# Kernel tuning notes

Measured on AMD Instinct MI355X. Metric: run time of the kernel, lower is better.

## Reference

```python
import jax, jax.numpy as jnp
import numpy as np

B, T, E = 4, 2048, 1024
H = 16
HS = E // H  # head_size = d_model // num_heads, d_model == E here
D_FF = 4 * E
EPS = 1e-5


def _layernorm(x, g, b):
    mu = jnp.mean(x, axis=-1, keepdims=True)
    var = jnp.var(x, axis=-1, keepdims=True)
    return (x - mu) * jax.lax.rsqrt(var + EPS) * g + b


def setup_inputs() -> dict:
    key = jax.random.key(0)
    ks = jax.random.split(key, 12)
    s_e = 1.0 / np.sqrt(E)
    s_ff = 1.0 / np.sqrt(D_FF)
    return {
        "x": jax.random.normal(ks[0], (B, T, E), jnp.float32),
        "ln1_g": jnp.ones((E,), jnp.float32),
        "ln1_b": jnp.zeros((E,), jnp.float32),
        "Wq": jax.random.normal(ks[1], (E, E), jnp.float32) * s_e,
        "bq": jnp.zeros((E,), jnp.float32),
        "Wk": jax.random.normal(ks[2], (E, E), jnp.float32) * s_e,
        "bk": jnp.zeros((E,), jnp.float32),
        "Wv": jax.random.normal(ks[3], (E, E), jnp.float32) * s_e,
        "bv": jnp.zeros((E,), jnp.float32),
        "Wp": jax.random.normal(ks[4], (E, E), jnp.float32) * s_e,
        "bp": jnp.zeros((E,), jnp.float32),
        "ln2_g": jnp.ones((E,), jnp.float32),
        "ln2_b": jnp.zeros((E,), jnp.float32),
        "W1": jax.random.normal(ks[5], (E, D_FF), jnp.float32) * s_e,
        "b1": jnp.zeros((D_FF,), jnp.float32),
        "W2": jax.random.normal(ks[6], (D_FF, E), jnp.float32) * s_ff,
        "b2": jnp.zeros((E,), jnp.float32),
    }


def reference(x, ln1_g, ln1_b, Wq, bq, Wk, bk, Wv, bv, Wp, bp,
              ln2_g, ln2_b, W1, b1, W2, b2):
    # --- attention sublayer ---
    h = _layernorm(x, ln1_g, ln1_b)                      # [B,T,E]
    q = (h @ Wq + bq).reshape(B, T, H, HS)
    k = (h @ Wk + bk).reshape(B, T, H, HS)
    v = (h @ Wv + bv).reshape(B, T, H, HS)
    scores = jnp.einsum('bqhd,bkhd->bhqk', q, k) * (HS ** -0.5)  # [B,H,T,T]
    causal = jnp.tril(jnp.ones((T, T), bool))
    scores = jnp.where(causal, scores, -jnp.inf)
    w = jax.nn.softmax(scores, axis=-1)
    attn = jnp.einsum('bhqk,bkhd->bqhd', w, v).reshape(B, T, H * HS)
    x = x + attn @ Wp + bp
    # --- FFN sublayer ---
    h2 = _layernorm(x, ln2_g, ln2_b)
    x = x + jax.nn.relu(h2 @ W1 + b1) @ W2 + b2
    return x
```

## Files before the change

### kernel.cpp

```cpp
#include <hip/hip_runtime.h>
#include <hip/hip_bf16.h>

#define B_ 4
#define T_ 2048
#define E_ 1024
#define H_ 16
#define HS_ 64
#define DFF_ 4096
#define M_ (B_ * T_)
#define LDQ_ (3 * E_)

typedef __bf16 bf16_t;
typedef __bf16 bf16x4 __attribute__((ext_vector_type(4)));
typedef __bf16 bf16x8 __attribute__((ext_vector_type(8)));
typedef float f32x4 __attribute__((ext_vector_type(4)));

#define AS1 __attribute__((address_space(1)))
#define AS3 __attribute__((address_space(3)))

__device__ __forceinline__ void gload_lds16(const void* g, void* l) {
  __builtin_amdgcn_global_load_lds((AS1 void*)(g), (AS3 void*)(l), 16, 0, 0);
}

__global__ __launch_bounds__(256) void wtrans_kernel(
    const float* __restrict__ W, bf16_t* __restrict__ Wt, int Krows, int Ncols) {
  __shared__ float tile[32][33];
  int tx = threadIdx.x, ty = threadIdx.y;
  int n0 = blockIdx.x * 32, k0 = blockIdx.y * 32;
#pragma unroll
  for (int i = 0; i < 32; i += 8)
    tile[ty + i][tx] = W[(long)(k0 + ty + i) * Ncols + n0 + tx];
  __syncthreads();
#pragma unroll
  for (int i = 0; i < 32; i += 8)
    Wt[(long)(n0 + ty + i) * Krows + k0 + tx] = (bf16_t)tile[tx][ty + i];
}

__global__ __launch_bounds__(256) void bcat_kernel(const float* a, const float* b,
                                                   const float* c, float* o) {
  int i = blockIdx.x * 256 + threadIdx.x;
  o[i] = i < 1024 ? a[i] : (i < 2048 ? b[i - 1024] : c[i - 2048]);
}

__global__ __launch_bounds__(256) void layernorm_kernel(
    const float* __restrict__ in, const float* __restrict__ g,
    const float* __restrict__ b, bf16_t* __restrict__ out) {
  int row = blockIdx.x;
  int tid = threadIdx.x;
  const float4* inr = (const float4*)(in + (long)row * E_);
  float4 v = inr[tid];
  float s = v.x + v.y + v.z + v.w;
  float ss = v.x * v.x + v.y * v.y + v.z * v.z + v.w * v.w;
#pragma unroll
  for (int o = 32; o; o >>= 1) {
    s += __shfl_xor(s, o);
    ss += __shfl_xor(ss, o);
  }
  __shared__ float red[8];
  int wv = tid >> 6;
  if ((tid & 63) == 0) {
    red[wv] = s;
    red[4 + wv] = ss;
  }
  __syncthreads();
  s = red[0] + red[1] + red[2] + red[3];
  ss = red[4] + red[5] + red[6] + red[7];
  float mu = s * (1.f / E_);
  float var = ss * (1.f / E_) - mu * mu;
  float rs = rsqrtf(var + 1e-5f);
  int ci = tid * 4;
  float4 gv = *(const float4*)(g + ci);
  float4 bv = *(const float4*)(b + ci);
  long o0 = (long)row * E_ + ci;
  out[o0 + 0] = (bf16_t)((v.x - mu) * rs * gv.x + bv.x);
  out[o0 + 1] = (bf16_t)((v.y - mu) * rs * gv.y + bv.y);
  out[o0 + 2] = (bf16_t)((v.z - mu) * rs * gv.z + bv.z);
  out[o0 + 3] = (bf16_t)((v.w - mu) * rs * gv.w + bv.w);
}

template <int RELU>
__global__ __launch_bounds__(512, 2) void gemm256_kernel(
    const bf16_t* __restrict__ A, const bf16_t* __restrict__ Bt,
    const float* __restrict__ bias, bf16_t* __restrict__ out, int N, int K) {
  __shared__ bf16_t As0[256 * 32], As1[256 * 32], As2[256 * 32], As3[256 * 32];
  __shared__ bf16_t Bs0[256 * 32], Bs1[256 * 32], Bs2[256 * 32], Bs3[256 * 32];
  const int tid = threadIdx.x;
  const int wave = tid >> 6;
  const int lane = tid & 63;
  const int wr = wave >> 2;
  const int wc = wave & 3;
  const int quad = lane >> 4, l16 = lane & 15;

  const int gx = gridDim.x;
  const int id = blockIdx.y * gx + blockIdx.x;
  const int xcd = id & 7;
  const int k_ = id >> 3;
  const int bxr = k_ % gx;
  const int byr = (k_ / gx) * 8 + xcd;
  const long rowBase = (long)byr * 256;
  const long colBase = (long)bxr * 256;

  f32x4 acc[8][4] = {};

  const int ntiles = K >> 5;

  auto stageA = [&](bf16_t* dst, int t) {
    const int k0 = t << 5;
#pragma unroll
    for (int p = 0; p < 2; ++p) {
      int idx = p * 512 + tid;
      int row = idx >> 2;
      int col = (idx & 3) * 8;
      gload_lds16(&A[(rowBase + row) * K + k0 + col],
                  dst + (p * 512 + wave * 64) * 8);
    }
  };
  auto stageB = [&](bf16_t* dst, int t) {
    const int k0 = t << 5;
#pragma unroll
    for (int p = 0; p < 2; ++p) {
      int idx = p * 512 + tid;
      int row = idx >> 2;
      int col = (idx & 3) * 8;
      gload_lds16(&Bt[(colBase + row) * K + k0 + col],
                  dst + (p * 512 + wave * 64) * 8);
    }
  };

  auto tileStep = [&](int t, const bf16_t* as, const bf16_t* bs, bf16_t* nA,
                      bf16_t* nB) {
    const bool pre = (t + 3 < ntiles);
    bf16x8 bfrag[4];
#pragma unroll
    for (int fc = 0; fc < 4; ++fc)
      bfrag[fc] = *(const bf16x8*)&bs[(wc * 64 + fc * 16 + l16) * 32 + quad * 8];

    {
      bf16x8 afrag[4];
#pragma unroll
      for (int fr = 0; fr < 4; ++fr)
        afrag[fr] =
            *(const bf16x8*)&as[(wr * 128 + fr * 16 + l16) * 32 + quad * 8];
      if (pre) stageA(nA, t + 3);
      __builtin_amdgcn_s_setprio(1);
#pragma unroll
      for (int fr = 0; fr < 4; ++fr)
#pragma unroll
        for (int fc = 0; fc < 4; ++fc)
          acc[fr][fc] = __builtin_amdgcn_mfma_f32_16x16x32_bf16(
              afrag[fr], bfrag[fc], acc[fr][fc], 0, 0, 0);
      __builtin_amdgcn_s_setprio(0);
      __builtin_amdgcn_s_barrier();
    }
    {
      bf16x8 afrag[4];
#pragma unroll
      for (int fr = 0; fr < 4; ++fr)
        afrag[fr] = *(const bf16x8*)&as[(wr * 128 + 64 + fr * 16 + l16) * 32 +
                                        quad * 8];
      if (pre) stageB(nB, t + 3);
      __builtin_amdgcn_s_setprio(1);
#pragma unroll
      for (int fr = 0; fr < 4; ++fr)
#pragma unroll
        for (int fc = 0; fc < 4; ++fc)
          acc[4 + fr][fc] = __builtin_amdgcn_mfma_f32_16x16x32_bf16(
              afrag[fr], bfrag[fc], acc[4 + fr][fc], 0, 0, 0);
      __builtin_amdgcn_s_setprio(0);
      if (t + 3 < ntiles)
        asm volatile("s_waitcnt vmcnt(8)" ::: "memory");
      else if (t + 2 < ntiles)
        asm volatile("s_waitcnt vmcnt(4)" ::: "memory");
      else if (t + 1 < ntiles)
        asm volatile("s_waitcnt vmcnt(0)" ::: "memory");
      if (t + 1 < ntiles) __builtin_amdgcn_s_barrier();
    }
  };

  stageA(As0, 0); stageB(Bs0, 0);
  stageA(As1, 1); stageB(Bs1, 1);
  stageA(As2, 2); stageB(Bs2, 2);
  asm volatile("s_waitcnt vmcnt(8)" ::: "memory");
  __builtin_amdgcn_s_barrier();

  for (int t = 0; t < ntiles; t += 4) {
    tileStep(t + 0, As0, Bs0, As3, Bs3);
    tileStep(t + 1, As1, Bs1, As0, Bs0);
    tileStep(t + 2, As2, Bs2, As1, Bs1);
    tileStep(t + 3, As3, Bs3, As2, Bs2);
  }

#pragma unroll
  for (int mh = 0; mh < 2; ++mh)
#pragma unroll
    for (int fr = 0; fr < 4; ++fr)
#pragma unroll
      for (int fc = 0; fc < 4; ++fc) {
        int colg = (int)colBase + wc * 64 + fc * 16 + l16;
        float bv = bias[colg];
#pragma unroll
        for (int r = 0; r < 4; ++r) {
          long rowg = rowBase + wr * 128 + mh * 64 + fr * 16 + quad * 4 + r;
          float v = acc[mh * 4 + fr][fc][r] + bv;
          if (RELU) v = fmaxf(v, 0.f);
          out[rowg * N + colg] = (bf16_t)v;
        }
      }
}

template <int MODE>
__global__ __launch_bounds__(512, 1) void gemm256x128_kernel(
    const bf16_t* __restrict__ A, const bf16_t* __restrict__ Bt,
    const float* __restrict__ bias, const float* __restrict__ resid,
    void* __restrict__ out, int N, int K) {
  __shared__ bf16_t As0[256 * 32], As1[256 * 32], As2[256 * 32], As3[256 * 32];
  __shared__ bf16_t Bs0[128 * 32], Bs1[128 * 32], Bs2[128 * 32], Bs3[128 * 32];
  const int tid = threadIdx.x;
  const int wave = tid >> 6;
  const int lane = tid & 63;
  const int wr = wave >> 1;
  const int wc = wave & 1;
  const int quad = lane >> 4, l16 = lane & 15;

  const int gx = gridDim.x;
  const int id = blockIdx.y * gx + blockIdx.x;
  const int xcd = id & 7;
  const int k_ = id >> 3;
  const int bxr = k_ % gx;
  const int byr = (k_ / gx) * 8 + xcd;
  const long rowBase = (long)byr * 256;
  const long colBase = (long)bxr * 128;

  f32x4 acc[4][4] = {};

  const int ntiles = K >> 5;

  auto stageA = [&](bf16_t* dst, int t) {
    const int k0 = t << 5;
#pragma unroll
    for (int p = 0; p < 2; ++p) {
      int idx = p * 512 + tid;
      int row = idx >> 2;
      int col = (idx & 3) * 8;
      gload_lds16(&A[(rowBase + row) * K + k0 + col],
                  dst + (p * 512 + wave * 64) * 8);
    }
  };
  auto stageB = [&](bf16_t* dst, int t) {
    const int k0 = t << 5;
    int row = tid >> 2;
    int col = (tid & 3) * 8;
    gload_lds16(&Bt[(colBase + row) * K + k0 + col], dst + (wave * 64) * 8);
  };

  auto tileStep = [&](int t, const bf16_t* as, const bf16_t* bs, bf16_t* nA,
                      bf16_t* nB) {
    const bool pre = (t + 3 < ntiles);
    bf16x8 bfrag[4];
#pragma unroll
    for (int fc = 0; fc < 4; ++fc)
      bfrag[fc] = *(const bf16x8*)&bs[(wc * 64 + fc * 16 + l16) * 32 + quad * 8];

    {
      bf16x8 afrag[2];
#pragma unroll
      for (int fr = 0; fr < 2; ++fr)
        afrag[fr] =
            *(const bf16x8*)&as[(wr * 64 + fr * 16 + l16) * 32 + quad * 8];
      if (pre) stageA(nA, t + 3);
      __builtin_amdgcn_s_setprio(1);
#pragma unroll
      for (int fr = 0; fr < 2; ++fr)
#pragma unroll
        for (int fc = 0; fc < 4; ++fc)
          acc[fr][fc] = __builtin_amdgcn_mfma_f32_16x16x32_bf16(
              afrag[fr], bfrag[fc], acc[fr][fc], 0, 0, 0);
      __builtin_amdgcn_s_setprio(0);
      __builtin_amdgcn_s_barrier();
    }
    {
      bf16x8 afrag[2];
#pragma unroll
      for (int fr = 2; fr < 4; ++fr)
        afrag[fr - 2] =
            *(const bf16x8*)&as[(wr * 64 + fr * 16 + l16) * 32 + quad * 8];
      if (pre) stageB(nB, t + 3);
      __builtin_amdgcn_s_setprio(1);
#pragma unroll
      for (int fr = 2; fr < 4; ++fr)
#pragma unroll
        for (int fc = 0; fc < 4; ++fc)
          acc[fr][fc] = __builtin_amdgcn_mfma_f32_16x16x32_bf16(
              afrag[fr - 2], bfrag[fc], acc[fr][fc], 0, 0, 0);
      __builtin_amdgcn_s_setprio(0);
      if (t + 3 < ntiles)
        asm volatile("s_waitcnt vmcnt(6)" ::: "memory");
      else if (t + 2 < ntiles)
        asm volatile("s_waitcnt vmcnt(3)" ::: "memory");
      else if (t + 1 < ntiles)
        asm volatile("s_waitcnt vmcnt(0)" ::: "memory");
      if (t + 1 < ntiles) __builtin_amdgcn_s_barrier();
    }
  };

  stageA(As0, 0); stageB(Bs0, 0);
  stageA(As1, 1); stageB(Bs1, 1);
  stageA(As2, 2); stageB(Bs2, 2);
  asm volatile("s_waitcnt vmcnt(6)" ::: "memory");
  __builtin_amdgcn_s_barrier();

  for (int t = 0; t < ntiles; t += 4) {
    tileStep(t + 0, As0, Bs0, As3, Bs3);
    tileStep(t + 1, As1, Bs1, As0, Bs0);
    tileStep(t + 2, As2, Bs2, As1, Bs1);
    tileStep(t + 3, As3, Bs3, As2, Bs2);
  }

#pragma unroll
  for (int fr = 0; fr < 4; ++fr)
#pragma unroll
    for (int fc = 0; fc < 4; ++fc) {
      int colg = (int)colBase + wc * 64 + fc * 16 + l16;
      float bv = bias[colg];
#pragma unroll
      for (int r = 0; r < 4; ++r) {
        long rowg = rowBase + wr * 64 + fr * 16 + quad * 4 + r;
        float v = acc[fr][fc][r] + bv;
        long idx = rowg * N + colg;
        if (MODE == 0) {
          ((bf16_t*)out)[idx] = (bf16_t)v;
        } else {
          ((float*)out)[idx] = v + resid[idx];
        }
      }
    }
}

__global__ __launch_bounds__(256) void vtrans_kernel(
    const bf16_t* __restrict__ qkv, bf16_t* __restrict__ vt) {
  __shared__ bf16_t tile[32][33];
  int tx = threadIdx.x, ty = threadIdx.y;
  int t0 = blockIdx.x * 32;
  int d0 = (blockIdx.y & 1) * 32;
  int bh = blockIdx.y >> 1;
  int b = bh >> 4, hh = bh & 15;
#pragma unroll
  for (int i = 0; i < 32; i += 8)
    tile[ty + i][tx] =
        qkv[(long)(b * T_ + t0 + ty + i) * LDQ_ + 2 * E_ + hh * HS_ + d0 + tx];
  __syncthreads();
#pragma unroll
  for (int i = 0; i < 32; i += 8)
    vt[((long)bh * HS_ + d0 + ty + i) * T_ + t0 + tx] = tile[tx][ty + i];
}

__global__ __launch_bounds__(256) void flash_attn_kernel(
    const bf16_t* __restrict__ qkv, const bf16_t* __restrict__ vt,
    bf16_t* __restrict__ attn, bf16_t* __restrict__ Opart,
    float* __restrict__ mlpart) {
  int gx = blockIdx.x;
  int ti = 0, sp = 0;
  for (int t = 0; t < 16; ++t) {
    int ns = t / 6 + 1;
    if (gx < ns) { ti = t; sp = gx; break; }
    gx -= ns;
  }
  const int nsplit = ti / 6 + 1;
  const int totIt = 2 * (ti + 1);
  const int jbeg = 12 * sp;
  const int jend = min(jbeg + 12, totIt);

  const int tid = threadIdx.x;
  const int lane = tid & 63, wave = tid >> 6;
  const int quad = lane >> 4, l16 = lane & 15;
  const int bh = blockIdx.y, b = bh >> 4, hh = bh & 15;
  const int q0 = ti * 128;
  const int qw = q0 + wave * 32;

  __shared__ __align__(16) bf16_t Ks[2][64 * 64];
  __shared__ __align__(16) bf16_t Vs[2][64 * 64];
  __shared__ __align__(16) bf16_t Ps[4][16 * 64];

  const bf16_t* qb = qkv;
  const bf16_t* kb = qkv + E_;

  bf16x8 aq[2][2];
#pragma unroll
  for (int s = 0; s < 2; ++s) {
    long base = (long)(b * T_ + qw + s * 16 + l16) * LDQ_ + hh * HS_ + quad * 8;
    aq[s][0] = *(const bf16x8*)&qb[base];
    aq[s][1] = *(const bf16x8*)&qb[base + 32];
#pragma unroll
    for (int e = 0; e < 8; ++e) {
      aq[s][0][e] = (bf16_t)((float)aq[s][0][e] * 0.125f);
      aq[s][1][e] = (bf16_t)((float)aq[s][1][e] * 0.125f);
    }
  }

  f32x4 o[2][4] = {};
  float lsum[2] = {};

  auto stage = [&](int buf, int j) {
    const int kv0 = j * 64;
#pragma unroll
    for (int i = 0; i < 2; ++i) {
      int c = i * 256 + tid;
      int row = c >> 3;
      int gcol = ((c & 7) ^ (row & 7)) * 8;
      gload_lds16(&kb[(long)(b * T_ + kv0 + row) * LDQ_ + hh * HS_ + gcol],
                  &Ks[buf][(i * 256 + wave * 64) * 8]);
      gload_lds16(&vt[((long)bh * HS_ + row) * T_ + kv0 + gcol],
                  &Vs[buf][(i * 256 + wave * 64) * 8]);
    }
  };

  stage(0, jbeg);
  __syncthreads();

  for (int j = jbeg; j < jend; ++j) {
    const int kv0 = j * 64;
    const int cur = (j - jbeg) & 1;
    if (j + 1 < jend) stage(cur ^ 1, j + 1);
    const bf16_t* KsL = Ks[cur];
    const bf16_t* VsL = Vs[cur];
    bf16_t* Pw = Ps[wave];

#pragma unroll
    for (int s = 0; s < 2; ++s) {
      const int qs = qw + s * 16;
      if (kv0 <= qs + 15) {
        f32x4 sc[4];
        __builtin_amdgcn_s_setprio(1);
#pragma unroll
        for (int sub = 0; sub < 4; ++sub) {
          const int rk = sub * 16 + l16;
          const int k0 = rk * 64 + ((quad ^ (rk & 7)) * 8);
          f32x4 t = {};
          t = __builtin_amdgcn_mfma_f32_16x16x32_bf16(
              *(const bf16x8*)&KsL[k0], aq[s][0], t, 0, 0, 0);
          t = __builtin_amdgcn_mfma_f32_16x16x32_bf16(
              *(const bf16x8*)&KsL[k0 ^ 32], aq[s][1], t, 0, 0, 0);
          sc[sub] = t;
        }
        __builtin_amdgcn_s_setprio(0);
        if (kv0 + 63 > qs) {
          int qcol = qs + l16;
#pragma unroll
          for (int sub = 0; sub < 4; ++sub)
#pragma unroll
            for (int r = 0; r < 4; ++r) {
              int kvrow = kv0 + sub * 16 + quad * 4 + r;
              if (kvrow > qcol) sc[sub][r] = -INFINITY;
            }
        }
        float part = 0.f;
#pragma unroll
        for (int sub = 0; sub < 4; ++sub) {
#pragma unroll
          for (int r = 0; r < 4; ++r) sc[sub][r] = __expf(sc[sub][r]);
          part += (sc[sub][0] + sc[sub][1]) + (sc[sub][2] + sc[sub][3]);
        }
        lsum[s] += part;
#pragma unroll
        for (int sub = 0; sub < 4; ++sub) {
          bf16x4 pk;
#pragma unroll
          for (int r = 0; r < 4; ++r) pk[r] = (bf16_t)sc[sub][r];
          const int ch = sub * 2 + (quad >> 1);
          const int off = ((ch ^ (l16 & 7)) * 8) + ((quad & 1) * 4);
          *(bf16x4*)&Pw[l16 * 64 + off] = pk;
        }
        const int p0 = l16 * 64 + ((quad ^ (l16 & 7)) * 8);
        bf16x8 ap0 = *(const bf16x8*)&Pw[p0];
        bf16x8 ap1 = *(const bf16x8*)&Pw[p0 ^ 32];
        __builtin_amdgcn_s_setprio(1);
#pragma unroll
        for (int nt = 0; nt < 4; ++nt) {
          const int rv = nt * 16 + l16;
          const int v0 = rv * 64 + ((quad ^ (rv & 7)) * 8);
          o[s][nt] = __builtin_amdgcn_mfma_f32_16x16x32_bf16(
              *(const bf16x8*)&VsL[v0], ap0, o[s][nt], 0, 0, 0);
          o[s][nt] = __builtin_amdgcn_mfma_f32_16x16x32_bf16(
              *(const bf16x8*)&VsL[v0 ^ 32], ap1, o[s][nt], 0, 0, 0);
        }
        __builtin_amdgcn_s_setprio(0);
      }
    }
    __syncthreads();
  }

  float lval[2];
#pragma unroll
  for (int s = 0; s < 2; ++s) {
    float v = lsum[s];
    v += __shfl_xor(v, 16);
    v += __shfl_xor(v, 32);
    lval[s] = v;
  }

  if (nsplit == 1) {
#pragma unroll
    for (int s = 0; s < 2; ++s) {
      float inv = 1.f / lval[s];
      long rowg = (long)b * T_ + qw + s * 16 + l16;
#pragma unroll
      for (int nt = 0; nt < 4; ++nt) {
        bf16x4 pk;
#pragma unroll
        for (int r = 0; r < 4; ++r) pk[r] = (bf16_t)(o[s][nt][r] * inv);
        *(bf16x4*)&attn[rowg * E_ + hh * HS_ + nt * 16 + quad * 4] = pk;
      }
    }
  } else {
    int idx = (ti < 12) ? (ti - 6) * 2 + sp : 12 + (ti - 12) * 3 + sp;
    long slot = (long)bh * 24 + idx;
    bf16_t* op = Opart + slot * (128 * 64);
    float* ml = mlpart + slot * 256;
#pragma unroll
    for (int s = 0; s < 2; ++s) {
      float inv = 1.f / lval[s];
      int rloc = wave * 32 + s * 16 + l16;
#pragma unroll
      for (int nt = 0; nt < 4; ++nt) {
        bf16x4 pk;
#pragma unroll
        for (int r = 0; r < 4; ++r) pk[r] = (bf16_t)(o[s][nt][r] * inv);
        *(bf16x4*)&op[rloc * 64 + nt * 16 + quad * 4] = pk;
      }
      if (quad == 0) ml[rloc] = lval[s];
    }
  }
}

__global__ __launch_bounds__(256) void flash_merge_kernel(
    const bf16_t* __restrict__ Opart, const float* __restrict__ mlpart,
    bf16_t* __restrict__ attn) {
  int ti = 6 + blockIdx.x;
  int bh = blockIdx.y, b = bh >> 4, hh = bh & 15;
  int ns = ti / 6 + 1;
  int base_idx = (ti < 12) ? (ti - 6) * 2 : 12 + (ti - 12) * 3;
  int r = threadIdx.x >> 1;
  int dh = (threadIdx.x & 1) * 32;

  float w[3], den = 0.f;
  for (int s = 0; s < ns; ++s) {
    long slot = (long)bh * 24 + base_idx + s;
    w[s] = mlpart[slot * 256 + r];
    den += w[s];
  }
  float inv = 1.f / den;
  float acc[32];
#pragma unroll
  for (int d = 0; d < 32; ++d) acc[d] = 0.f;
  for (int s = 0; s < ns; ++s) {
    long slot = (long)bh * 24 + base_idx + s;
    const bf16_t* op = Opart + slot * (128 * 64) + r * 64 + dh;
#pragma unroll
    for (int d = 0; d < 32; ++d) acc[d] += w[s] * (float)op[d];
  }
  long rowg = (long)b * T_ + ti * 128 + r;
  bf16_t* dst = attn + rowg * E_ + hh * HS_ + dh;
#pragma unroll
  for (int d = 0; d < 32; ++d) dst[d] = (bf16_t)(acc[d] * inv);
}

extern "C" void kernel_launch(void* const* d_in, const int* in_sizes, int n_in,
                              void* d_out, int out_size, void* d_ws,
                              size_t ws_size, hipStream_t stream) {
  const float* x = (const float*)d_in[0];
  const float* ln1_g = (const float*)d_in[1];
  const float* ln1_b = (const float*)d_in[2];
  const float* Wq = (const float*)d_in[3];
  const float* bq = (const float*)d_in[4];
  const float* Wk = (const float*)d_in[5];
  const float* bk = (const float*)d_in[6];
  const float* Wv = (const float*)d_in[7];
  const float* bv = (const float*)d_in[8];
  const float* Wp = (const float*)d_in[9];
  const float* bp = (const float*)d_in[10];
  const float* ln2_g = (const float*)d_in[11];
  const float* ln2_b = (const float*)d_in[12];
  const float* W1 = (const float*)d_in[13];
  const float* b1 = (const float*)d_in[14];
  const float* W2 = (const float*)d_in[15];
  const float* b2 = (const float*)d_in[16];
  float* out = (float*)d_out;

  const size_t MB = 1ull << 20;
  char* ws = (char*)d_ws;
  bf16_t* wqkvt = (bf16_t*)(ws + 0 * MB);
  bf16_t* wpt   = (bf16_t*)(ws + 6 * MB);
  bf16_t* w1t   = (bf16_t*)(ws + 8 * MB);
  bf16_t* w2t   = (bf16_t*)(ws + 16 * MB);
  float*  bqkv  = (float*)(ws + 24 * MB);
  bf16_t* h     = (bf16_t*)(ws + 25 * MB);
  bf16_t* qkvb  = (bf16_t*)(ws + 41 * MB);
  bf16_t* vt    = (bf16_t*)(ws + 89 * MB);
  float*  xmid  = (float*)(ws + 105 * MB);
  bf16_t* Opart = (bf16_t*)(ws + 105 * MB);
  float* mlpart = (float*)(ws + 131 * MB);
  bf16_t* attn  = h;
  bf16_t* h2    = h;
  bf16_t* ff1   = qkvb;

  dim3 tb(32, 8);
  wtrans_kernel<<<dim3(E_ / 32, E_ / 32), tb, 0, stream>>>(Wq, wqkvt, E_, E_);
  wtrans_kernel<<<dim3(E_ / 32, E_ / 32), tb, 0, stream>>>(Wk, wqkvt + (long)E_ * E_, E_, E_);
  wtrans_kernel<<<dim3(E_ / 32, E_ / 32), tb, 0, stream>>>(Wv, wqkvt + 2l * E_ * E_, E_, E_);
  wtrans_kernel<<<dim3(E_ / 32, E_ / 32), tb, 0, stream>>>(Wp, wpt, E_, E_);
  wtrans_kernel<<<dim3(DFF_ / 32, E_ / 32), tb, 0, stream>>>(W1, w1t, E_, DFF_);
  wtrans_kernel<<<dim3(E_ / 32, DFF_ / 32), tb, 0, stream>>>(W2, w2t, DFF_, E_);
  bcat_kernel<<<12, 256, 0, stream>>>(bq, bk, bv, bqkv);

  layernorm_kernel<<<M_, 256, 0, stream>>>(x, ln1_g, ln1_b, h);

  gemm256x128_kernel<0><<<dim3(3 * E_ / 128, M_ / 256), 512, 0, stream>>>(
      h, wqkvt, bqkv, nullptr, qkvb, 3 * E_, E_);

  vtrans_kernel<<<dim3(T_ / 32, 2 * B_ * H_), tb, 0, stream>>>(qkvb, vt);

  flash_attn_kernel<<<dim3(30, B_ * H_), 256, 0, stream>>>(qkvb, vt, attn,
                                                           Opart, mlpart);
  flash_merge_kernel<<<dim3(10, B_ * H_), 256, 0, stream>>>(Opart, mlpart, attn);

  gemm256x128_kernel<1><<<dim3(E_ / 128, M_ / 256), 512, 0, stream>>>(
      attn, wpt, bp, x, xmid, E_, E_);

  layernorm_kernel<<<M_, 256, 0, stream>>>(xmid, ln2_g, ln2_b, h2);

  gemm256_kernel<1><<<dim3(DFF_ / 256, M_ / 256), 512, 0, stream>>>(
      h2, w1t, b1, ff1, DFF_, E_);
  gemm256x128_kernel<1><<<dim3(E_ / 128, M_ / 256), 512, 0, stream>>>(
      ff1, w2t, b2, xmid, out, E_, DFF_);
}
```

Baseline: 505.0 us.

## Triple-buffer K/V tiles in attention with prefetch depth two and vmcnt waits

Replaces the double-buffered K/V shared-memory staging in the causal attention kernel with three rotating buffers. Each step prefetches the tile two iterations ahead. It replaces the full __syncthreads with a partial s_waitcnt vmcnt plus a raw s_barrier, so loads can stay in flight across iterations. This is meant to hide global-to-LDS latency better, at the cost of more LDS per block (possible occupancy loss) and more fragile hand-written wait counts.

```diff
diff --git a/kernel.cpp b/kernel.cpp
--- a/kernel.cpp
+++ b/kernel.cpp
@@ -377,8 +377,8 @@
   const int q0 = ti * 128;
   const int qw = q0 + wave * 32;
 
-  __shared__ __align__(16) bf16_t Ks[2][64 * 64];
-  __shared__ __align__(16) bf16_t Vs[2][64 * 64];
+  __shared__ __align__(16) bf16_t K0s[64 * 64], K1s[64 * 64], K2s[64 * 64];
+  __shared__ __align__(16) bf16_t V0s[64 * 64], V1s[64 * 64], V2s[64 * 64];
   __shared__ __align__(16) bf16_t Ps[4][16 * 64];
 
   const bf16_t* qb = qkv;
@@ -400,7 +400,7 @@
   f32x4 o[2][4] = {};
   float lsum[2] = {};
 
-  auto stage = [&](int buf, int j) {
+  auto stage = [&](bf16_t* Kd, bf16_t* Vd, int j) {
     const int kv0 = j * 64;
 #pragma unroll
     for (int i = 0; i < 2; ++i) {
@@ -408,21 +408,16 @@
       int row = c >> 3;
       int gcol = ((c & 7) ^ (row & 7)) * 8;
       gload_lds16(&kb[(long)(b * T_ + kv0 + row) * LDQ_ + hh * HS_ + gcol],
-                  &Ks[buf][(i * 256 + wave * 64) * 8]);
+                  Kd + (i * 256 + wave * 64) * 8);
       gload_lds16(&vt[((long)bh * HS_ + row) * T_ + kv0 + gcol],
-                  &Vs[buf][(i * 256 + wave * 64) * 8]);
-    }
-  };
-
-  stage(0, jbeg);
-  __syncthreads();
-
-  for (int j = jbeg; j < jend; ++j) {
+                  Vd + (i * 256 + wave * 64) * 8);
+    }
+  };
+
+  auto step = [&](int j, const bf16_t* KsL, const bf16_t* VsL, bf16_t* pK,
+                  bf16_t* pV) {
+    if (j + 2 < jend) stage(pK, pV, j + 2);
     const int kv0 = j * 64;
-    const int cur = (j - jbeg) & 1;
-    if (j + 1 < jend) stage(cur ^ 1, j + 1);
-    const bf16_t* KsL = Ks[cur];
-    const bf16_t* VsL = Vs[cur];
     bf16_t* Pw = Ps[wave];
 
 #pragma unroll
@@ -486,7 +481,27 @@
         __builtin_amdgcn_s_setprio(0);
       }
     }
-    __syncthreads();
+    if (j + 2 < jend)
+      asm volatile("s_waitcnt vmcnt(4)" ::: "memory");
+    else if (j + 1 < jend)
+      asm volatile("s_waitcnt vmcnt(0)" ::: "memory");
+    if (j + 1 < jend) __builtin_amdgcn_s_barrier();
+  };
+
+  stage(K0s, V0s, jbeg);
+  if (jbeg + 1 < jend) {
+    stage(K1s, V1s, jbeg + 1);
+    asm volatile("s_waitcnt vmcnt(4)" ::: "memory");
+  } else {
+    asm volatile("s_waitcnt vmcnt(0)" ::: "memory");
+  }
+  __builtin_amdgcn_s_barrier();
+
+  int j = jbeg;
+  while (true) {
+    step(j, K0s, V0s, K2s, V2s); if (++j >= jend) break;
+    step(j, K1s, V1s, K0s, V0s); if (++j >= jend) break;
+    step(j, K2s, V2s, K1s, V1s); if (++j >= jend) break;
   }
 
   float lval[2];
```

New measurement: 528.4 us. 4.6% more time.

## Fuse V transpose into QKV GEMM epilogue and pair query tiles per flash block

Applied to the files above, without the earlier changes.

The QKV GEMM epilogue now also writes the V columns in transposed [bh, d, t] layout, which removes the separate vtrans kernel launch and its extra read and write of V. The flash attention kernel moves to 512 threads, with two query tiles (2p and 2p+1) sharing each staged K/V block, so grid x drops from 30 to 15 and K/V loads are reused across both tiles. The transposed stores in the epilogue are strided and uncoalesced. The paired half-blocks also carry unequal causal work, so waves in the shorter tile may idle during its masked iterations.

```diff
diff --git a/kernel.cpp b/kernel.cpp
--- a/kernel.cpp
+++ b/kernel.cpp
@@ -212,7 +212,7 @@
 __global__ __launch_bounds__(512, 1) void gemm256x128_kernel(
     const bf16_t* __restrict__ A, const bf16_t* __restrict__ Bt,
     const float* __restrict__ bias, const float* __restrict__ resid,
-    void* __restrict__ out, int N, int K) {
+    void* __restrict__ out, bf16_t* __restrict__ vt_out, int N, int K) {
   __shared__ bf16_t As0[256 * 32], As1[256 * 32], As2[256 * 32], As3[256 * 32];
   __shared__ bf16_t Bs0[128 * 32], Bs1[128 * 32], Bs2[128 * 32], Bs3[128 * 32];
   const int tid = threadIdx.x;
@@ -327,59 +327,51 @@
         long rowg = rowBase + wr * 64 + fr * 16 + quad * 4 + r;
         float v = acc[fr][fc][r] + bv;
         long idx = rowg * N + colg;
-        if (MODE == 0) {
+        if (MODE == 1) {
+          ((float*)out)[idx] = v + resid[idx];
+        } else {
           ((bf16_t*)out)[idx] = (bf16_t)v;
-        } else {
-          ((float*)out)[idx] = v + resid[idx];
+          if (MODE == 2 && colg >= 2 * E_) {
+            int d = colg & 63;
+            int hh2 = (colg - 2 * E_) >> 6;
+            int bb = (int)(rowg >> 11);
+            int tt = (int)(rowg & 2047);
+            vt_out[(((long)(bb * 16 + hh2)) * 64 + d) * T_ + tt] = (bf16_t)v;
+          }
         }
       }
     }
 }
 
-__global__ __launch_bounds__(256) void vtrans_kernel(
-    const bf16_t* __restrict__ qkv, bf16_t* __restrict__ vt) {
-  __shared__ bf16_t tile[32][33];
-  int tx = threadIdx.x, ty = threadIdx.y;
-  int t0 = blockIdx.x * 32;
-  int d0 = (blockIdx.y & 1) * 32;
-  int bh = blockIdx.y >> 1;
-  int b = bh >> 4, hh = bh & 15;
-#pragma unroll
-  for (int i = 0; i < 32; i += 8)
-    tile[ty + i][tx] =
-        qkv[(long)(b * T_ + t0 + ty + i) * LDQ_ + 2 * E_ + hh * HS_ + d0 + tx];
-  __syncthreads();
-#pragma unroll
-  for (int i = 0; i < 32; i += 8)
-    vt[((long)bh * HS_ + d0 + ty + i) * T_ + t0 + tx] = tile[tx][ty + i];
-}
-
-__global__ __launch_bounds__(256) void flash_attn_kernel(
+__global__ __launch_bounds__(512) void flash_attn_kernel(
     const bf16_t* __restrict__ qkv, const bf16_t* __restrict__ vt,
     bf16_t* __restrict__ attn, bf16_t* __restrict__ Opart,
     float* __restrict__ mlpart) {
-  int gx = blockIdx.x;
-  int ti = 0, sp = 0;
-  for (int t = 0; t < 16; ++t) {
-    int ns = t / 6 + 1;
-    if (gx < ns) { ti = t; sp = gx; break; }
+  int gx = 14 - (int)blockIdx.x;
+  int pt = 0, sp = 0;
+  for (int p = 0; p < 8; ++p) {
+    int ns = (2 * p + 1) / 6 + 1;
+    if (gx < ns) { pt = p; sp = gx; break; }
     gx -= ns;
   }
-  const int nsplit = ti / 6 + 1;
-  const int totIt = 2 * (ti + 1);
-  const int jbeg = 12 * sp;
-  const int jend = min(jbeg + 12, totIt);
 
   const int tid = threadIdx.x;
-  const int lane = tid & 63, wave = tid >> 6;
+  const int wave = tid >> 6;
+  const int half = wave >> 2;
+  const int wsub = wave & 3;
+  const int lane = tid & 63;
   const int quad = lane >> 4, l16 = lane & 15;
   const int bh = blockIdx.y, b = bh >> 4, hh = bh & 15;
-  const int q0 = ti * 128;
-  const int qw = q0 + wave * 32;
+
+  const int ti = 2 * pt + half;
+  const int nsplit = ti / 6 + 1;
+  const int qw = ti * 128 + wsub * 32;
+  const int jbeg = 12 * sp;
+  const int jendU = min(12 * sp + 12, 4 * pt + 4);
 
   __shared__ __align__(16) bf16_t Ks[2][64 * 64];
   __shared__ __align__(16) bf16_t Vs[2][64 * 64];
-  __shared__ __align__(16) bf16_t Ps[4][16 * 64];
+  __shared__ __align__(16) bf16_t Ps[8][16 * 64];
 
   const bf16_t* qb = qkv;
   const bf16_t* kb = qkv + E_;
@@ -402,25 +394,21 @@
 
   auto stage = [&](int buf, int j) {
     const int kv0 = j * 64;
-#pragma unroll
-    for (int i = 0; i < 2; ++i) {
-      int c = i * 256 + tid;
-      int row = c >> 3;
-      int gcol = ((c & 7) ^ (row & 7)) * 8;
-      gload_lds16(&kb[(long)(b * T_ + kv0 + row) * LDQ_ + hh * HS_ + gcol],
-                  &Ks[buf][(i * 256 + wave * 64) * 8]);
-      gload_lds16(&vt[((long)bh * HS_ + row) * T_ + kv0 + gcol],
-                  &Vs[buf][(i * 256 + wave * 64) * 8]);
-    }
+    int row = tid >> 3;
+    int gcol = ((tid & 7) ^ (row & 7)) * 8;
+    gload_lds16(&kb[(long)(b * T_ + kv0 + row) * LDQ_ + hh * HS_ + gcol],
+                &Ks[buf][wave * 512]);
+    gload_lds16(&vt[((long)bh * HS_ + row) * T_ + kv0 + gcol],
+                &Vs[buf][wave * 512]);
   };
 
   stage(0, jbeg);
   __syncthreads();
 
-  for (int j = jbeg; j < jend; ++j) {
+  for (int j = jbeg; j < jendU; ++j) {
     const int kv0 = j * 64;
     const int cur = (j - jbeg) & 1;
-    if (j + 1 < jend) stage(cur ^ 1, j + 1);
+    if (j + 1 < jendU) stage(cur ^ 1, j + 1);
     const bf16_t* KsL = Ks[cur];
     const bf16_t* VsL = Vs[cur];
     bf16_t* Pw = Ps[wave];
@@ -519,7 +507,7 @@
 #pragma unroll
     for (int s = 0; s < 2; ++s) {
       float inv = 1.f / lval[s];
-      int rloc = wave * 32 + s * 16 + l16;
+      int rloc = wsub * 32 + s * 16 + l16;
 #pragma unroll
       for (int nt = 0; nt < 4; ++nt) {
         bf16x4 pk;
@@ -614,22 +602,20 @@
 
   layernorm_kernel<<<M_, 256, 0, stream>>>(x, ln1_g, ln1_b, h);
 
-  gemm256x128_kernel<0><<<dim3(3 * E_ / 128, M_ / 256), 512, 0, stream>>>(
-      h, wqkvt, bqkv, nullptr, qkvb, 3 * E_, E_);
-
-  vtrans_kernel<<<dim3(T_ / 32, 2 * B_ * H_), tb, 0, stream>>>(qkvb, vt);
-
-  flash_attn_kernel<<<dim3(30, B_ * H_), 256, 0, stream>>>(qkvb, vt, attn,
+  gemm256x128_kernel<2><<<dim3(3 * E_ / 128, M_ / 256), 512, 0, stream>>>(
+      h, wqkvt, bqkv, nullptr, qkvb, vt, 3 * E_, E_);
+
+  flash_attn_kernel<<<dim3(15, B_ * H_), 512, 0, stream>>>(qkvb, vt, attn,
                                                            Opart, mlpart);
   flash_merge_kernel<<<dim3(10, B_ * H_), 256, 0, stream>>>(Opart, mlpart, attn);
 
   gemm256x128_kernel<1><<<dim3(E_ / 128, M_ / 256), 512, 0, stream>>>(
-      attn, wpt, bp, x, xmid, E_, E_);
+      attn, wpt, bp, x, xmid, nullptr, E_, E_);
 
   layernorm_kernel<<<M_, 256, 0, stream>>>(xmid, ln2_g, ln2_b, h2);
 
   gemm256_kernel<1><<<dim3(DFF_ / 256, M_ / 256), 512, 0, stream>>>(
       h2, w1t, b1, ff1, DFF_, E_);
   gemm256x128_kernel<1><<<dim3(E_ / 128, M_ / 256), 512, 0, stream>>>(
-      ff1, w2t, b2, xmid, out, E_, DFF_);
-}
+      ff1, w2t, b2, xmid, out, nullptr, E_, DFF_);
+}
```

Result: no change. 512.3 us (+1.4%).
